# Optimization experiments

Measured on AMD Instinct MI355X. Metric: run time of the kernel, lower is better.

## Reference

```python
import jax, jax.numpy as jnp
import numpy as np

N, K, F_IN, F_OUT = 32768, 16, 128, 128
NEG_SLOPE = 0.2  # LeakyReLU slope in original module


def setup_inputs() -> dict:
    key = jax.random.key(0)
    ks = jax.random.split(key, 8)
    nodes = jax.random.normal(ks[0], (N, F_IN), dtype=jnp.float32)
    neighbors = jax.random.normal(ks[1], (N, K, F_IN), dtype=jnp.float32)
    aspects = jax.random.normal(ks[2], (N, K, F_IN), dtype=jnp.float32)
    attention_scores = jax.random.uniform(ks[3], (N, K), dtype=jnp.float32)
    # Parameters (torch.nn.Linear stores weight as [out, in])
    lim_w = float(np.sqrt(6.0 / (F_IN + F_OUT)))  # xavier_uniform
    W = jax.random.uniform(ks[4], (F_OUT, F_IN), minval=-lim_w, maxval=lim_w, dtype=jnp.float32)
    lim_a = float(np.sqrt(6.0 / (2 * F_IN + F_OUT)))
    Wa = jax.random.uniform(ks[5], (F_OUT, 2 * F_IN), minval=-lim_a, maxval=lim_a, dtype=jnp.float32)
    ba = jax.random.uniform(ks[6], (F_OUT,), minval=-0.05, maxval=0.05, dtype=jnp.float32)
    bias = jnp.zeros((F_OUT,), dtype=jnp.float32)
    return {"nodes": nodes, "neighbors": neighbors, "aspects": aspects,
            "attention_scores": attention_scores, "W": W, "Wa": Wa, "ba": ba, "bias": bias}


def reference(nodes, neighbors, aspects, attention_scores, W, Wa, ba, bias):
    # linear_proj (no bias); dropout(p=0.01) treated as eval/identity
    node_proj = nodes @ W.T                                  # [N, F_OUT]
    neigh_proj = jnp.einsum('nkf,of->nko', neighbors, W)     # [N, K, F_OUT]
    asp_proj = jnp.einsum('nkf,of->nko', aspects, W)         # [N, K, F_OUT]
    # aspects_method == 'linear': cat(neigh_proj, asp_proj) then Linear(2F->F)
    cat = jnp.concatenate([neigh_proj, asp_proj], axis=-1)   # [N, K, 2*F_OUT]
    nap = jnp.einsum('nkf,of->nko', cat, Wa) + ba            # [N, K, F_OUT]
    # per-edge: leakyReLU(nap + broadcast target node proj).exp()
    features_per_edge = jnp.exp(jax.nn.leaky_relu(nap + node_proj[:, None, :], NEG_SLOPE))
    # weight by attention score and sum over neighbors (scatter-sum per node)
    out = jnp.sum(features_per_edge * attention_scores[..., None], axis=1)  # [N, F_OUT]
    # skip_concat_bias: concat=True -> view [N, F_OUT], add bias, ELU activation
    return jax.nn.elu(out + bias)
```

## Files before the change

kernel.cpp:

```cpp
#include <hip/hip_runtime.h>
#include <hip/hip_bf16.h>
#include <stdint.h>

typedef short bf16x8 __attribute__((ext_vector_type(8)));
typedef float f32x4  __attribute__((ext_vector_type(4)));
typedef float f32x2  __attribute__((ext_vector_type(2)));

#define NNODES    32768
#define KNB       16
#define FDIM      128
#define KTOT      384
#define NEG_SLOPE 0.2f

static __device__ __forceinline__ unsigned short f2bf(float x) {
  union { float f; unsigned u; } v; v.f = x;
  unsigned r = v.u + 0x7fffu + ((v.u >> 16) & 1u);
  return (unsigned short)(r >> 16);
}

static __device__ __forceinline__ bf16x8 pack8(f32x4 lo, f32x4 hi) {
  union { __hip_bfloat162 h[4]; bf16x8 v; } u;
  u.h[0] = __float22bfloat162_rn(make_float2(lo[0], lo[1]));
  u.h[1] = __float22bfloat162_rn(make_float2(lo[2], lo[3]));
  u.h[2] = __float22bfloat162_rn(make_float2(hi[0], hi[1]));
  u.h[3] = __float22bfloat162_rn(make_float2(hi[2], hi[3]));
  return u.v;
}

__global__ void prep_weights(const float* __restrict__ W,
                             const float* __restrict__ Wa,
                             unsigned short* __restrict__ Bmat) {
  const int o = blockIdx.x;
  const int f = threadIdx.x;
  const float* war = Wa + o * 256;
  float a1 = 0.f, a2 = 0.f;
  #pragma unroll 8
  for (int j = 0; j < 128; ++j) {
    float w = W[j * 128 + f];
    a1 = fmaf(war[j], w, a1);
    a2 = fmaf(war[128 + j], w, a2);
  }
  Bmat[o * KTOT + f]       = f2bf(a1);
  Bmat[o * KTOT + 128 + f] = f2bf(a2);
  Bmat[o * KTOT + 256 + f] = f2bf(W[o * 128 + f]);
}

__global__ void grn_main(const float* __restrict__ nodes,
                         const float* __restrict__ neighbors,
                         const float* __restrict__ aspects,
                         const float* __restrict__ scores,
                         const unsigned short* __restrict__ Bmat,
                         const float* __restrict__ ba,
                         const float* __restrict__ bias,
                         float* __restrict__ out) {
  const int lane = threadIdx.x & 63;
  const int wv   = threadIdx.x >> 6;
  const int quad = lane >> 4;
  const int l16  = lane & 15;
  const int n0   = blockIdx.x * 8 + wv * 2;

  __shared__ float xpose[4][2][FDIM];

  bf16x8 afrag[2][12];
  #pragma unroll
  for (int i = 0; i < 2; ++i) {
    const int n = n0 + i;
    const float* nb = neighbors + ((size_t)n * KNB + l16) * FDIM;
    const float* as = aspects   + ((size_t)n * KNB + l16) * FDIM;
    const float* nd = nodes     + (size_t)n * FDIM;
    #pragma unroll
    for (int h = 0; h < 2; ++h) {
      f32x4 lo[6], hi[6];
      #pragma unroll
      for (int j = 0; j < 6; ++j) {
        const int kc  = h * 6 + j;
        const int seg = kc >> 2;
        const int fo  = (kc & 3) * 32 + quad * 8;
        const float* src = (seg == 0) ? nb + fo : (seg == 1) ? as + fo : nd + fo;
        lo[j] = *(const f32x4*)src;
        hi[j] = *(const f32x4*)(src + 4);
      }
      #pragma unroll
      for (int j = 0; j < 6; ++j) afrag[i][h * 6 + j] = pack8(lo[j], hi[j]);
    }
  }

  f32x4 acc[2][8];
  #pragma unroll
  for (int i = 0; i < 2; ++i)
    #pragma unroll
    for (int ct = 0; ct < 8; ++ct)
      acc[i][ct] = (f32x4){0.f, 0.f, 0.f, 0.f};

  #pragma unroll
  for (int kc = 0; kc < 12; ++kc) {
    const unsigned short* bbase = Bmat + (size_t)l16 * KTOT + kc * 32 + quad * 8;
    #pragma unroll
    for (int ct = 0; ct < 8; ++ct) {
      bf16x8 bfrag = *(const bf16x8*)(bbase + (size_t)(ct * 16) * KTOT);
      acc[0][ct] = __builtin_amdgcn_mfma_f32_16x16x32_bf16(afrag[0][kc], bfrag, acc[0][ct], 0, 0, 0);
      acc[1][ct] = __builtin_amdgcn_mfma_f32_16x16x32_bf16(afrag[1][kc], bfrag, acc[1][ct], 0, 0, 0);
    }
  }

  #pragma unroll
  for (int i = 0; i < 2; ++i) {
    const int n = n0 + i;
    f32x4 sc = *(const f32x4*)(scores + (size_t)n * KNB + quad * 4);
    #pragma unroll
    for (int ct = 0; ct < 8; ++ct) {
      const int c = ct * 16 + l16;
      const float bav = ba[c];
      float s = 0.f;
      #pragma unroll
      for (int r = 0; r < 4; ++r) {
        float t  = acc[i][ct][r] + bav;
        float lr = t > 0.f ? t : NEG_SLOPE * t;
        s = fmaf(__expf(lr), sc[r], s);
      }
      s += __shfl_xor(s, 16);
      s += __shfl_xor(s, 32);
      if ((ct & 3) == quad) xpose[wv][i][c] = s;
    }
  }
  __syncthreads();

  #pragma unroll
  for (int i = 0; i < 2; ++i) {
    f32x2 sv = *(const f32x2*)&xpose[wv][i][2 * lane];
    f32x2 bv = *(const f32x2*)(bias + 2 * lane);
    float v0 = sv[0] + bv[0];
    float v1 = sv[1] + bv[1];
    v0 = v0 > 0.f ? v0 : (__expf(v0) - 1.f);
    v1 = v1 > 0.f ? v1 : (__expf(v1) - 1.f);
    *(f32x2*)(out + (size_t)(n0 + i) * FDIM + 2 * lane) = (f32x2){v0, v1};
  }
}

extern "C" void kernel_launch(void* const* d_in, const int* in_sizes, int n_in,
                              void* d_out, int out_size, void* d_ws, size_t ws_size,
                              hipStream_t stream) {
  const float* nodes     = (const float*)d_in[0];
  const float* neighbors = (const float*)d_in[1];
  const float* aspects   = (const float*)d_in[2];
  const float* scores    = (const float*)d_in[3];
  const float* W         = (const float*)d_in[4];
  const float* Wa        = (const float*)d_in[5];
  const float* ba        = (const float*)d_in[6];
  const float* bias      = (const float*)d_in[7];
  unsigned short* Bmat   = (unsigned short*)d_ws;

  prep_weights<<<128, 128, 0, stream>>>(W, Wa, Bmat);
  grn_main<<<NNODES / 8, 256, 0, stream>>>(nodes, neighbors, aspects, scores,
                                           Bmat, ba, bias, (float*)d_out);
}
```

Before: 676.7 us.

## Persistent blocks with register-resident weights and double-buffered LDS staging of edges

Replaces the per-wave reload of the full fused weight matrix with a persistent kernel. Each wave keeps one output-column tile of the weights in registers, with the weights pre-laid out in fragment order by the prep kernel. Edge features are loaded cooperatively, converted to bf16 and staged in swizzled, double-buffered shared memory, with the next node pair prefetched while the current one is computed. This removes redundant weight traffic, at the cost of a per-iteration block barrier and limited prefetch depth.

```diff
diff --git a/kernel.cpp b/kernel.cpp
--- a/kernel.cpp
+++ b/kernel.cpp
@@ -4,13 +4,13 @@
 
 typedef short bf16x8 __attribute__((ext_vector_type(8)));
 typedef float f32x4  __attribute__((ext_vector_type(4)));
-typedef float f32x2  __attribute__((ext_vector_type(2)));
 
 #define NNODES    32768
 #define KNB       16
 #define FDIM      128
-#define KTOT      384
 #define NEG_SLOPE 0.2f
+#define NBLK      512
+#define PPB       (NNODES / (2 * NBLK))
 
 static __device__ __forceinline__ unsigned short f2bf(float x) {
   union { float f; unsigned u; } v; v.f = x;
@@ -27,9 +27,15 @@
   return u.v;
 }
 
+static __device__ __forceinline__ void storeBL(unsigned short* BL, int ct, int l16,
+                                               int col, unsigned short v) {
+  const int kc = col >> 5, quad = (col >> 3) & 3, j = col & 7;
+  BL[(size_t)(((kc * 8 + ct) * 64) + quad * 16 + l16) * 8 + j] = v;
+}
+
 __global__ void prep_weights(const float* __restrict__ W,
                              const float* __restrict__ Wa,
-                             unsigned short* __restrict__ Bmat) {
+                             unsigned short* __restrict__ BL) {
   const int o = blockIdx.x;
   const int f = threadIdx.x;
   const float* war = Wa + o * 256;
@@ -40,100 +46,145 @@
     a1 = fmaf(war[j], w, a1);
     a2 = fmaf(war[128 + j], w, a2);
   }
-  Bmat[o * KTOT + f]       = f2bf(a1);
-  Bmat[o * KTOT + 128 + f] = f2bf(a2);
-  Bmat[o * KTOT + 256 + f] = f2bf(W[o * 128 + f]);
-}
-
-__global__ void grn_main(const float* __restrict__ nodes,
-                         const float* __restrict__ neighbors,
-                         const float* __restrict__ aspects,
-                         const float* __restrict__ scores,
-                         const unsigned short* __restrict__ Bmat,
-                         const float* __restrict__ ba,
-                         const float* __restrict__ bias,
-                         float* __restrict__ out) {
-  const int lane = threadIdx.x & 63;
-  const int wv   = threadIdx.x >> 6;
+  const int ct = o >> 4, l16 = o & 15;
+  storeBL(BL, ct, l16, f,       f2bf(a1));
+  storeBL(BL, ct, l16, 128 + f, f2bf(a2));
+  storeBL(BL, ct, l16, 256 + f, f2bf(W[o * 128 + f]));
+}
+
+__global__ __launch_bounds__(512, 4)
+void grn_main(const float* __restrict__ nodes,
+              const float* __restrict__ neighbors,
+              const float* __restrict__ aspects,
+              const float* __restrict__ scores,
+              const unsigned short* __restrict__ BL,
+              const float* __restrict__ ba,
+              const float* __restrict__ bias,
+              float* __restrict__ out) {
+  const int tid  = threadIdx.x;
+  const int lane = tid & 63;
+  const int w    = tid >> 6;
   const int quad = lane >> 4;
   const int l16  = lane & 15;
-  const int n0   = blockIdx.x * 8 + wv * 2;
-
-  __shared__ float xpose[4][2][FDIM];
-
-  bf16x8 afrag[2][12];
+
+  __shared__ __align__(16) unsigned short Aeg[2][8192];
+  __shared__ __align__(16) unsigned short And[2][256];
+  __shared__ float xp[2][2][FDIM];
+
+  bf16x8 breg[12];
   #pragma unroll
-  for (int i = 0; i < 2; ++i) {
-    const int n = n0 + i;
-    const float* nb = neighbors + ((size_t)n * KNB + l16) * FDIM;
-    const float* as = aspects   + ((size_t)n * KNB + l16) * FDIM;
-    const float* nd = nodes     + (size_t)n * FDIM;
-    #pragma unroll
-    for (int h = 0; h < 2; ++h) {
-      f32x4 lo[6], hi[6];
-      #pragma unroll
-      for (int j = 0; j < 6; ++j) {
-        const int kc  = h * 6 + j;
-        const int seg = kc >> 2;
-        const int fo  = (kc & 3) * 32 + quad * 8;
-        const float* src = (seg == 0) ? nb + fo : (seg == 1) ? as + fo : nd + fo;
-        lo[j] = *(const f32x4*)src;
-        hi[j] = *(const f32x4*)(src + 4);
-      }
-      #pragma unroll
-      for (int j = 0; j < 6; ++j) afrag[i][h * 6 + j] = pack8(lo[j], hi[j]);
-    }
+  for (int kc = 0; kc < 12; ++kc)
+    breg[kc] = *(const bf16x8*)(BL + ((size_t)(kc * 8 + w) * 64 + lane) * 8);
+
+  const float ba_c = ba[w * 16 + l16];
+  float bias_t = 0.f;
+  if (tid < 256) bias_t = bias[tid & 127];
+
+  const int seg = tid >> 8;
+  const int row = (tid >> 4) & 15;
+  const int c16 = tid & 15;
+  const int cc  = seg * 16 + c16;
+  const float* segp = seg ? aspects : neighbors;
+  const int wroff = row * 512 + ((cc * 16) ^ ((row & 7) << 4));
+  const int sw    = (l16 & 7) << 4;
+  const int rdrow = l16 * 512;
+
+  const int pair0 = blockIdx.x * PPB;
+
+  f32x4 eg[2][2];
+  f32x4 nd[2];
+
+  {
+    const size_t ng = (size_t)pair0 * 2;
+    #pragma unroll
+    for (int n = 0; n < 2; ++n) {
+      const float* src = segp + ((ng + n) * KNB + row) * FDIM + c16 * 8;
+      eg[n][0] = *(const f32x4*)src;
+      eg[n][1] = *(const f32x4*)(src + 4);
+    }
+    if (tid < 32) {
+      const float* nsrc = nodes + (ng + (tid >> 4)) * FDIM + (tid & 15) * 8;
+      nd[0] = *(const f32x4*)nsrc;
+      nd[1] = *(const f32x4*)(nsrc + 4);
+    }
+    #pragma unroll
+    for (int n = 0; n < 2; ++n)
+      *(bf16x8*)((char*)Aeg[0] + n * 8192 + wroff) = pack8(eg[n][0], eg[n][1]);
+    if (tid < 32)
+      *(bf16x8*)((char*)And[0] + tid * 16) = pack8(nd[0], nd[1]);
   }
-
-  f32x4 acc[2][8];
-  #pragma unroll
-  for (int i = 0; i < 2; ++i)
-    #pragma unroll
-    for (int ct = 0; ct < 8; ++ct)
-      acc[i][ct] = (f32x4){0.f, 0.f, 0.f, 0.f};
-
-  #pragma unroll
-  for (int kc = 0; kc < 12; ++kc) {
-    const unsigned short* bbase = Bmat + (size_t)l16 * KTOT + kc * 32 + quad * 8;
-    #pragma unroll
-    for (int ct = 0; ct < 8; ++ct) {
-      bf16x8 bfrag = *(const bf16x8*)(bbase + (size_t)(ct * 16) * KTOT);
-      acc[0][ct] = __builtin_amdgcn_mfma_f32_16x16x32_bf16(afrag[0][kc], bfrag, acc[0][ct], 0, 0, 0);
-      acc[1][ct] = __builtin_amdgcn_mfma_f32_16x16x32_bf16(afrag[1][kc], bfrag, acc[1][ct], 0, 0, 0);
-    }
-  }
-
-  #pragma unroll
-  for (int i = 0; i < 2; ++i) {
-    const int n = n0 + i;
-    f32x4 sc = *(const f32x4*)(scores + (size_t)n * KNB + quad * 4);
-    #pragma unroll
-    for (int ct = 0; ct < 8; ++ct) {
-      const int c = ct * 16 + l16;
-      const float bav = ba[c];
+  __syncthreads();
+
+  for (int i = 0; i < PPB; ++i) {
+    const int buf = i & 1;
+    const size_t ng = (size_t)(pair0 + i) * 2;
+
+    if (i + 1 < PPB) {
+      const size_t ng2 = ng + 2;
+      #pragma unroll
+      for (int n = 0; n < 2; ++n) {
+        const float* src = segp + ((ng2 + n) * KNB + row) * FDIM + c16 * 8;
+        eg[n][0] = *(const f32x4*)src;
+        eg[n][1] = *(const f32x4*)(src + 4);
+      }
+      if (tid < 32) {
+        const float* nsrc = nodes + (ng2 + (tid >> 4)) * FDIM + (tid & 15) * 8;
+        nd[0] = *(const f32x4*)nsrc;
+        nd[1] = *(const f32x4*)(nsrc + 4);
+      }
+    }
+
+    f32x4 acc[2];
+    acc[0] = (f32x4){0.f, 0.f, 0.f, 0.f};
+    acc[1] = (f32x4){0.f, 0.f, 0.f, 0.f};
+    const char* ab = (const char*)Aeg[buf];
+    const char* nb = (const char*)And[buf];
+    #pragma unroll
+    for (int n = 0; n < 2; ++n) {
+      #pragma unroll
+      for (int kc = 0; kc < 8; ++kc) {
+        bf16x8 af = *(const bf16x8*)(ab + n * 8192 + rdrow +
+                                     (((kc * 4 + quad) * 16) ^ sw));
+        acc[n] = __builtin_amdgcn_mfma_f32_16x16x32_bf16(af, breg[kc], acc[n], 0, 0, 0);
+      }
+      #pragma unroll
+      for (int kn = 0; kn < 4; ++kn) {
+        bf16x8 af = *(const bf16x8*)(nb + (n * 16 + kn * 4 + quad) * 16);
+        acc[n] = __builtin_amdgcn_mfma_f32_16x16x32_bf16(af, breg[8 + kn], acc[n], 0, 0, 0);
+      }
+    }
+
+    #pragma unroll
+    for (int n = 0; n < 2; ++n) {
+      f32x4 sc = *(const f32x4*)(scores + (ng + n) * KNB + quad * 4);
       float s = 0.f;
       #pragma unroll
       for (int r = 0; r < 4; ++r) {
-        float t  = acc[i][ct][r] + bav;
+        float t  = acc[n][r] + ba_c;
         float lr = t > 0.f ? t : NEG_SLOPE * t;
         s = fmaf(__expf(lr), sc[r], s);
       }
       s += __shfl_xor(s, 16);
       s += __shfl_xor(s, 32);
-      if ((ct & 3) == quad) xpose[wv][i][c] = s;
-    }
-  }
-  __syncthreads();
-
-  #pragma unroll
-  for (int i = 0; i < 2; ++i) {
-    f32x2 sv = *(const f32x2*)&xpose[wv][i][2 * lane];
-    f32x2 bv = *(const f32x2*)(bias + 2 * lane);
-    float v0 = sv[0] + bv[0];
-    float v1 = sv[1] + bv[1];
-    v0 = v0 > 0.f ? v0 : (__expf(v0) - 1.f);
-    v1 = v1 > 0.f ? v1 : (__expf(v1) - 1.f);
-    *(f32x2*)(out + (size_t)(n0 + i) * FDIM + 2 * lane) = (f32x2){v0, v1};
+      if (quad == 0) xp[buf][n][w * 16 + l16] = s;
+    }
+
+    if (i + 1 < PPB) {
+      const int nbuf = buf ^ 1;
+      #pragma unroll
+      for (int n = 0; n < 2; ++n)
+        *(bf16x8*)((char*)Aeg[nbuf] + n * 8192 + wroff) = pack8(eg[n][0], eg[n][1]);
+      if (tid < 32)
+        *(bf16x8*)((char*)And[nbuf] + tid * 16) = pack8(nd[0], nd[1]);
+    }
+    __syncthreads();
+
+    if (tid < 256) {
+      const int n = tid >> 7, c = tid & 127;
+      float v = xp[buf][n][c] + bias_t;
+      v = v > 0.f ? v : __expf(v) - 1.f;
+      out[(ng + n) * FDIM + c] = v;
+    }
   }
 }
 
@@ -148,9 +199,9 @@
   const float* Wa        = (const float*)d_in[5];
   const float* ba        = (const float*)d_in[6];
   const float* bias      = (const float*)d_in[7];
-  unsigned short* Bmat   = (unsigned short*)d_ws;
-
-  prep_weights<<<128, 128, 0, stream>>>(W, Wa, Bmat);
-  grn_main<<<NNODES / 8, 256, 0, stream>>>(nodes, neighbors, aspects, scores,
-                                           Bmat, ba, bias, (float*)d_out);
-}
+  unsigned short* BL     = (unsigned short*)d_ws;
+
+  prep_weights<<<128, 128, 0, stream>>>(W, Wa, BL);
+  grn_main<<<NBLK, 512, 0, stream>>>(nodes, neighbors, aspects, scores,
+                                     BL, ba, bias, (float*)d_out);
+}
```

Result: faster. 547.1 us (-19.2%).
